# Kernel optimization log

Measured on AMD Instinct MI355X. Metric: run time of the kernel, lower is better.

Reference implementation:

```python
import jax, jax.numpy as jnp
import numpy as np

N = 50000
DIM = 768   # input_dim == feature dim (self.L)
D_ATT = 128 # self.D


def setup_inputs() -> dict:
    key = jax.random.key(0)
    ks = jax.random.split(key, 6)
    s = lambda fan_in: 1.0 / np.sqrt(fan_in)
    return {
        "x": jax.random.normal(ks[0], (1, N, DIM), dtype=jnp.float32),
        "W_feat": jax.random.normal(ks[1], (DIM, DIM), dtype=jnp.float32) * s(DIM),
        "b_feat": jax.random.normal(ks[2], (DIM,), dtype=jnp.float32) * s(DIM),
        "W_a": jax.random.normal(ks[3], (D_ATT, DIM), dtype=jnp.float32) * s(DIM),
        "W_b": jax.random.normal(ks[4], (D_ATT, DIM), dtype=jnp.float32) * s(DIM),
        "W_c": jax.random.normal(ks[5], (1, D_ATT), dtype=jnp.float32) * s(D_ATT),
    }


def reference(x, W_feat, b_feat, W_a, W_b, W_c):
    # x: [1, N, DIM] -> squeeze bag dim -> [N, DIM]
    h = jax.nn.relu(jnp.einsum('nd,ed->ne', x[0], W_feat) + b_feat)  # [N, 768]
    a = jax.nn.relu(jnp.einsum('nd,kd->nk', h, W_a))      # [N, 128]
    b = jax.nn.sigmoid(jnp.einsum('nd,kd->nk', h, W_b))   # [N, 128]
    logits = jnp.einsum('nk,ok->on', a * b, W_c)           # [1, N] (transpose fused)
    A = jax.nn.softmax(logits, axis=-1)                    # [1, N]
    return jnp.einsum('on,nd->od', A, h)                   # [1, 768]
```

## Files before the change

### kernel.cpp

```cpp
#include <hip/hip_runtime.h>
#include <hip/hip_bf16.h>
#include <stdint.h>

#define DEVINL __device__ __forceinline__

using bf16x8 = __attribute__((ext_vector_type(8))) short;
using f32x4  = __attribute__((ext_vector_type(4))) float;

static constexpr int NPTS = 50000;
static constexpr int NPAD = 50176;
static constexpr int DIM  = 768;
static constexpr int DATT = 128;
static constexpr int NRB  = NPAD / 128;

DEVINL ushort f2b(float f) {
  uint32_t u = __float_as_uint(f);
  u += 0x7fffu + ((u >> 16) & 1u);
  return (ushort)(u >> 16);
}
DEVINL float b2f(ushort u) { return __uint_as_float(((uint32_t)u) << 16); }

DEVINL void gload_lds16(const void* g, void* l) {
  __builtin_amdgcn_global_load_lds((const __attribute__((address_space(1))) void*)g,
                                   (__attribute__((address_space(3))) void*)l,
                                   16, 0, 0);
}

DEVINL uint32_t cvtpk(float lo, float hi) {
  union { __hip_bfloat162 h2; uint32_t u; } c;
  c.h2 = __float22bfloat162_rn(float2{lo, hi});
  return c.u;
}
DEVINL bf16x8 pack8(f32x4 lo, f32x4 hi) {
  union { uint32_t u[4]; bf16x8 v; } r;
  r.u[0] = cvtpk(lo[0], lo[1]);
  r.u[1] = cvtpk(lo[2], lo[3]);
  r.u[2] = cvtpk(hi[0], hi[1]);
  r.u[3] = cvtpk(hi[2], hi[3]);
  return r.v;
}

__global__ void cvt_weights_kernel(const float* __restrict__ Wf, const float* __restrict__ Wa,
                                   const float* __restrict__ Wb,
                                   ushort* __restrict__ wfb, ushort* __restrict__ wab,
                                   ushort* __restrict__ wbb) {
  const int NF = DIM * DIM / 8, NA = DATT * DIM / 8;
  int i = blockIdx.x * blockDim.x + threadIdx.x;
  const float* src; ushort* dst; int j;
  if (i < NF)               { src = Wf; dst = wfb; j = i; }
  else if (i < NF + NA)     { src = Wa; dst = wab; j = i - NF; }
  else if (i < NF + 2 * NA) { src = Wb; dst = wbb; j = i - NF - NA; }
  else return;
  const float4* s4 = (const float4*)src;
  float4 v0 = s4[(long)j * 2];
  float4 v1 = s4[(long)j * 2 + 1];
  ushort4 o0 = { f2b(v0.x), f2b(v0.y), f2b(v0.z), f2b(v0.w) };
  ushort4 o1 = { f2b(v1.x), f2b(v1.y), f2b(v1.z), f2b(v1.w) };
  ((ushort4*)dst)[(long)j * 2]     = o0;
  ((ushort4*)dst)[(long)j * 2 + 1] = o1;
}

__global__ __launch_bounds__(512, 2)
void gemm_h_fused(const float* __restrict__ X, const ushort* __restrict__ Wfb,
                  const float* __restrict__ bias, ushort* __restrict__ H) {
  __shared__ char lds[2][65536];

  const int tid  = threadIdx.x;
  const int wid  = tid >> 6;
  const int lane = tid & 63;

  const int bid  = blockIdx.x;
  const int wgid = (bid & 7) * 147 + (bid >> 3);
  const int row0 = (wgid / 3) * 128;
  const int col0 = (wgid % 3) * 256;

  const int wrow = (wid >> 2) * 64;
  const int wcol = (wid & 3) * 64;

  f32x4 acc[4][4] = {};

  const int rA   = wid * 4 + (lane >> 4);
  const int swzA = ((lane & 15) ^ (rA & 7)) * 4;
  const int rB   = wid * 8 + (lane >> 3);
  const int swzB = ((lane & 7) ^ (rB & 7)) * 8;

  auto STAGE = [&](int t, int buf) {
    const int k0 = t * 64;
    char* base = &lds[buf][0];
#pragma unroll
    for (int i = 0; i < 4; ++i) {
      const int r  = i * 32 + rA;
      const int rg = row0 + r;
      const int src = rg < NPTS ? rg : NPTS - 1;
      gload_lds16(X + (long)src * DIM + k0 + swzA, base + (i * 32 + wid * 4) * 256);
    }
#pragma unroll
    for (int i = 0; i < 4; ++i) {
      const int r = i * 64 + rB;
      gload_lds16(Wfb + (long)(col0 + r) * DIM + k0 + swzB,
                  base + 32768 + (i * 64 + wid * 8) * 128);
    }
  };

  auto COMPUTE = [&](int buf) {
    const float*  Ab = (const float*)&lds[buf][0];
    const ushort* Bb = (const ushort*)&lds[buf][32768];
#pragma unroll
    for (int kk = 0; kk < 2; ++kk) {
      const int j = kk * 4 + (lane >> 4);
      bf16x8 a[4];
#pragma unroll
      for (int m = 0; m < 4; ++m) {
        const int ra = wrow + m * 16 + (lane & 15);
        const int s  = ra & 7;
        f32x4 lo = *(const f32x4*)(Ab + ra * 64 + (((2 * j)     ^ s) << 2));
        f32x4 hi = *(const f32x4*)(Ab + ra * 64 + (((2 * j + 1) ^ s) << 2));
        a[m] = pack8(lo, hi);
      }
#pragma unroll
      for (int n = 0; n < 4; ++n) {
        const int rb = wcol + n * 16 + (lane & 15);
        bf16x8 b = *(const bf16x8*)(Bb + rb * 64 + ((j ^ (rb & 7)) << 3));
#pragma unroll
        for (int m = 0; m < 4; ++m)
          acc[m][n] = __builtin_amdgcn_mfma_f32_16x16x32_bf16(a[m], b, acc[m][n], 0, 0, 0);
      }
    }
  };

  STAGE(0, 0);
  asm volatile("s_waitcnt vmcnt(0)" ::: "memory");
  __builtin_amdgcn_s_barrier();
  __builtin_amdgcn_sched_barrier(0);

#pragma unroll 1
  for (int t = 0; t < 12; ++t) {
    if (t < 11) STAGE(t + 1, (t + 1) & 1);
    __builtin_amdgcn_sched_barrier(0);
    COMPUTE(t & 1);
    asm volatile("s_waitcnt vmcnt(0)" ::: "memory");
    __builtin_amdgcn_s_barrier();
    __builtin_amdgcn_sched_barrier(0);
  }

  const int lq = lane >> 4;
  const int lc = lane & 15;
#pragma unroll
  for (int n = 0; n < 4; ++n) {
    const int cg = col0 + wcol + n * 16 + lc;
    const float bv = bias[cg];
#pragma unroll
    for (int m = 0; m < 4; ++m) {
      const int rg = row0 + wrow + m * 16 + lq * 4;
#pragma unroll
      for (int r2 = 0; r2 < 4; ++r2) {
        float v = acc[m][n][r2] + bv;
        v = fmaxf(v, 0.0f);
        H[(long)(rg + r2) * DIM + cg] = f2b(v);
      }
    }
  }
}

__global__ __launch_bounds__(512)
void gate_kernel(const ushort* __restrict__ Hm, const ushort* __restrict__ Wa,
                 const ushort* __restrict__ Wb, const float* __restrict__ Wc,
                 float* __restrict__ logits) {
  __shared__ ushort Hs [128 * 64];
  __shared__ ushort Was[128 * 64];
  __shared__ ushort Wbs[128 * 64];
  const int tid  = threadIdx.x;
  const int wid  = tid >> 6;
  const int lane = tid & 63;
  const int row0 = blockIdx.x * 128;

  f32x4 fa[8] = {};
  f32x4 fb[8] = {};

  const int ld_r = lane >> 3;
  const int ld_c = (lane & 7) * 8;

  for (int k0 = 0; k0 < DIM; k0 += 64) {
    __syncthreads();
#pragma unroll
    for (int i = 0; i < 2; ++i) {
      const int ch = i * 8 + wid;
      const int r  = ch * 8 + ld_r;
      gload_lds16(Hm + (long)(row0 + r) * DIM + k0 + ld_c, Hs  + ch * 512);
      gload_lds16(Wa + (long)r * DIM        + k0 + ld_c, Was + ch * 512);
      gload_lds16(Wb + (long)r * DIM        + k0 + ld_c, Wbs + ch * 512);
    }
    __syncthreads();
#pragma unroll
    for (int kk = 0; kk < 2; ++kk) {
      const int kc = kk * 32 + (lane >> 4) * 8;
      bf16x8 h = *(const bf16x8*)(Hs + (wid * 16 + (lane & 15)) * 64 + kc);
#pragma unroll
      for (int n = 0; n < 8; ++n) {
        bf16x8 wa = *(const bf16x8*)(Was + (n * 16 + (lane & 15)) * 64 + kc);
        bf16x8 wb = *(const bf16x8*)(Wbs + (n * 16 + (lane & 15)) * 64 + kc);
        fa[n] = __builtin_amdgcn_mfma_f32_16x16x32_bf16(h, wa, fa[n], 0, 0, 0);
        fb[n] = __builtin_amdgcn_mfma_f32_16x16x32_bf16(h, wb, fb[n], 0, 0, 0);
      }
    }
  }

  const int lc = lane & 15;
  const int lq = lane >> 4;
  float g[4];
#pragma unroll
  for (int r = 0; r < 4; ++r) {
    float s = 0.f;
#pragma unroll
    for (int n = 0; n < 8; ++n) {
      float av = fmaxf(fa[n][r], 0.f);
      float sg = 1.f / (1.f + expf(-fb[n][r]));
      s += av * sg * Wc[n * 16 + lc];
    }
    s += __shfl_xor(s, 1);
    s += __shfl_xor(s, 2);
    s += __shfl_xor(s, 4);
    s += __shfl_xor(s, 8);
    g[r] = s;
  }
  if (lc == 0) {
    const int rbase = row0 + wid * 16 + lq * 4;
#pragma unroll
    for (int r = 0; r < 4; ++r) {
      const int nidx = rbase + r;
      if (nidx < NPTS) logits[nidx] = g[r];
    }
  }
}

__global__ __launch_bounds__(1024)
void softmax_stats_kernel(const float* __restrict__ logits, float* __restrict__ stats) {
  __shared__ float red[1024];
  const int tid = threadIdx.x;
  float m = -1e30f;
  for (int i = tid; i < NPTS; i += 1024) m = fmaxf(m, logits[i]);
  red[tid] = m; __syncthreads();
  for (int s = 512; s > 0; s >>= 1) {
    if (tid < s) red[tid] = fmaxf(red[tid], red[tid + s]);
    __syncthreads();
  }
  m = red[0];
  __syncthreads();
  float sum = 0.f;
  for (int i = tid; i < NPTS; i += 1024) sum += expf(logits[i] - m);
  red[tid] = sum; __syncthreads();
  for (int s = 512; s > 0; s >>= 1) {
    if (tid < s) red[tid] += red[tid + s];
    __syncthreads();
  }
  if (tid == 0) { stats[0] = m; stats[1] = red[0]; }
}

__global__ __launch_bounds__(192)
void weighted_partial_kernel(const ushort* __restrict__ Hm, const float* __restrict__ logits,
                             const float* __restrict__ stats, float* __restrict__ part) {
  __shared__ float w[128];
  const int b = blockIdx.x, tid = threadIdx.x;
  const int n0 = b * 128;
  if (tid < 128) {
    const int n = n0 + tid;
    w[tid] = (n < NPTS) ? expf(logits[n] - stats[0]) : 0.f;
  }
  __syncthreads();
  float4 acc = {0.f, 0.f, 0.f, 0.f};
  const ushort* hp = Hm + (long)n0 * DIM + tid * 4;
#pragma unroll 4
  for (int r = 0; r < 128; ++r) {
    const float wr = w[r];
    ushort4 v = *(const ushort4*)(hp + (long)r * DIM);
    acc.x += wr * b2f(v.x);
    acc.y += wr * b2f(v.y);
    acc.z += wr * b2f(v.z);
    acc.w += wr * b2f(v.w);
  }
  ((float4*)(part + (long)b * DIM))[tid] = acc;
}

__global__ void final_reduce_kernel(const float* __restrict__ part,
                                    const float* __restrict__ stats,
                                    float* __restrict__ out) {
  const int c = blockIdx.x * blockDim.x + threadIdx.x;
  if (c >= DIM) return;
  float s = 0.f;
  for (int b = 0; b < NRB; ++b) s += part[(long)b * DIM + c];
  out[c] = s / stats[1];
}

extern "C" void kernel_launch(void* const* d_in, const int* in_sizes, int n_in,
                              void* d_out, int out_size, void* d_ws, size_t ws_size,
                              hipStream_t stream) {
  const float* x  = (const float*)d_in[0];
  const float* Wf = (const float*)d_in[1];
  const float* bf = (const float*)d_in[2];
  const float* Wa = (const float*)d_in[3];
  const float* Wb = (const float*)d_in[4];
  const float* Wc = (const float*)d_in[5];
  float* out = (float*)d_out;

  char* p = (char*)d_ws;
  ushort* hb  = (ushort*)p; p += (size_t)NPAD * DIM * 2;
  ushort* wfb = (ushort*)p; p += (size_t)DIM * DIM * 2;
  ushort* wab = (ushort*)p; p += (size_t)DATT * DIM * 2;
  ushort* wbb = (ushort*)p; p += (size_t)DATT * DIM * 2;
  float* logits = (float*)p; p += (size_t)NPAD * 4;
  float* stats  = (float*)p; p += 256;
  float* part   = (float*)p; p += (size_t)NRB * DIM * 4;

  cvt_weights_kernel<<<384, 256, 0, stream>>>(Wf, Wa, Wb, wfb, wab, wbb);

  gemm_h_fused<<<392 * 3, 512, 0, stream>>>(x, wfb, bf, hb);
  gate_kernel<<<NRB, 512, 0, stream>>>(hb, wab, wbb, Wc, logits);
  softmax_stats_kernel<<<1, 1024, 0, stream>>>(logits, stats);
  weighted_partial_kernel<<<NRB, 192, 0, stream>>>(hb, logits, stats, part);
  final_reduce_kernel<<<3, 256, 0, stream>>>(part, stats, out);
}
```

Before: 220.0 us.

## Shrink GEMM tiles with triple-buffered LDS pipeline and parallelize softmax stats

The feature GEMM switches from 128x256 to 128x128 output tiles, doubling the grid, and replaces double buffering with a three-stage LDS ring that keeps two loads in flight using partial vmcnt waits. The single-block softmax statistics kernel is split into a 49-block partial max/sum pass followed by a one-wave combine kernel. The aim is better latency hiding and occupancy in the GEMM and removing a serial bottleneck in the softmax reduction. The trade-off is more A-tile reloads across column tiles, lower MFMA work per LDS read, and one extra kernel launch.

```diff
diff --git a/kernel.cpp b/kernel.cpp
--- a/kernel.cpp
+++ b/kernel.cpp
@@ -12,6 +12,7 @@
 static constexpr int DIM  = 768;
 static constexpr int DATT = 128;
 static constexpr int NRB  = NPAD / 128;
+static constexpr int NSMB = 49;
 
 DEVINL ushort f2b(float f) {
   uint32_t u = __float_as_uint(f);
@@ -60,24 +61,24 @@
   ((ushort4*)dst)[(long)j * 2 + 1] = o1;
 }
 
-__global__ __launch_bounds__(512, 2)
+__global__ __launch_bounds__(512)
 void gemm_h_fused(const float* __restrict__ X, const ushort* __restrict__ Wfb,
                   const float* __restrict__ bias, ushort* __restrict__ H) {
-  __shared__ char lds[2][65536];
+  __shared__ char lds[3][49152];
 
   const int tid  = threadIdx.x;
   const int wid  = tid >> 6;
   const int lane = tid & 63;
 
   const int bid  = blockIdx.x;
-  const int wgid = (bid & 7) * 147 + (bid >> 3);
-  const int row0 = (wgid / 3) * 128;
-  const int col0 = (wgid % 3) * 256;
-
-  const int wrow = (wid >> 2) * 64;
-  const int wcol = (wid & 3) * 64;
-
-  f32x4 acc[4][4] = {};
+  const int wgid = (bid & 7) * 294 + (bid >> 3);
+  const int row0 = (wgid / 6) * 128;
+  const int col0 = (wgid % 6) * 128;
+
+  const int wrow = (wid >> 1) * 32;
+  const int wcol = (wid & 1) * 64;
+
+  f32x4 acc[2][4] = {};
 
   const int rA   = wid * 4 + (lane >> 4);
   const int swzA = ((lane & 15) ^ (rA & 7)) * 4;
@@ -89,13 +90,12 @@
     char* base = &lds[buf][0];
 #pragma unroll
     for (int i = 0; i < 4; ++i) {
-      const int r  = i * 32 + rA;
-      const int rg = row0 + r;
+      const int rg  = row0 + i * 32 + rA;
       const int src = rg < NPTS ? rg : NPTS - 1;
       gload_lds16(X + (long)src * DIM + k0 + swzA, base + (i * 32 + wid * 4) * 256);
     }
 #pragma unroll
-    for (int i = 0; i < 4; ++i) {
+    for (int i = 0; i < 2; ++i) {
       const int r = i * 64 + rB;
       gload_lds16(Wfb + (long)(col0 + r) * DIM + k0 + swzB,
                   base + 32768 + (i * 64 + wid * 8) * 128);
@@ -108,9 +108,9 @@
 #pragma unroll
     for (int kk = 0; kk < 2; ++kk) {
       const int j = kk * 4 + (lane >> 4);
-      bf16x8 a[4];
-#pragma unroll
-      for (int m = 0; m < 4; ++m) {
+      bf16x8 a[2];
+#pragma unroll
+      for (int m = 0; m < 2; ++m) {
         const int ra = wrow + m * 16 + (lane & 15);
         const int s  = ra & 7;
         f32x4 lo = *(const f32x4*)(Ab + ra * 64 + (((2 * j)     ^ s) << 2));
@@ -122,25 +122,32 @@
         const int rb = wcol + n * 16 + (lane & 15);
         bf16x8 b = *(const bf16x8*)(Bb + rb * 64 + ((j ^ (rb & 7)) << 3));
 #pragma unroll
-        for (int m = 0; m < 4; ++m)
+        for (int m = 0; m < 2; ++m)
           acc[m][n] = __builtin_amdgcn_mfma_f32_16x16x32_bf16(a[m], b, acc[m][n], 0, 0, 0);
       }
     }
   };
 
   STAGE(0, 0);
-  asm volatile("s_waitcnt vmcnt(0)" ::: "memory");
-  __builtin_amdgcn_s_barrier();
-  __builtin_amdgcn_sched_barrier(0);
-
+  STAGE(1, 1);
+  int c = 0;
 #pragma unroll 1
   for (int t = 0; t < 12; ++t) {
-    if (t < 11) STAGE(t + 1, (t + 1) & 1);
-    __builtin_amdgcn_sched_barrier(0);
-    COMPUTE(t & 1);
-    asm volatile("s_waitcnt vmcnt(0)" ::: "memory");
+    if (t < 10) {
+      const int nb = (c == 0) ? 2 : c - 1;
+      STAGE(t + 2, nb);
+      asm volatile("s_waitcnt vmcnt(12)" ::: "memory");
+    } else if (t == 10) {
+      asm volatile("s_waitcnt vmcnt(6)" ::: "memory");
+    } else {
+      asm volatile("s_waitcnt vmcnt(0)" ::: "memory");
+    }
     __builtin_amdgcn_s_barrier();
     __builtin_amdgcn_sched_barrier(0);
+    COMPUTE(c);
+    __builtin_amdgcn_sched_barrier(0);
+    __builtin_amdgcn_s_barrier();
+    c = (c == 2) ? 0 : c + 1;
   }
 
   const int lq = lane >> 4;
@@ -150,7 +157,7 @@
     const int cg = col0 + wcol + n * 16 + lc;
     const float bv = bias[cg];
 #pragma unroll
-    for (int m = 0; m < 4; ++m) {
+    for (int m = 0; m < 2; ++m) {
       const int rg = row0 + wrow + m * 16 + lq * 4;
 #pragma unroll
       for (int r2 = 0; r2 < 4; ++r2) {
@@ -234,26 +241,37 @@
 }
 
 __global__ __launch_bounds__(1024)
-void softmax_stats_kernel(const float* __restrict__ logits, float* __restrict__ stats) {
+void softmax_part_kernel(const float* __restrict__ logits, float* __restrict__ part2) {
   __shared__ float red[1024];
   const int tid = threadIdx.x;
-  float m = -1e30f;
-  for (int i = tid; i < NPTS; i += 1024) m = fmaxf(m, logits[i]);
-  red[tid] = m; __syncthreads();
+  const int n = blockIdx.x * 1024 + tid;
+  const float v = (n < NPTS) ? logits[n] : -1e30f;
+  red[tid] = v; __syncthreads();
   for (int s = 512; s > 0; s >>= 1) {
     if (tid < s) red[tid] = fmaxf(red[tid], red[tid + s]);
     __syncthreads();
   }
-  m = red[0];
+  const float m = red[0];
   __syncthreads();
-  float sum = 0.f;
-  for (int i = tid; i < NPTS; i += 1024) sum += expf(logits[i] - m);
-  red[tid] = sum; __syncthreads();
+  red[tid] = (n < NPTS) ? expf(v - m) : 0.f;
+  __syncthreads();
   for (int s = 512; s > 0; s >>= 1) {
     if (tid < s) red[tid] += red[tid + s];
     __syncthreads();
   }
-  if (tid == 0) { stats[0] = m; stats[1] = red[0]; }
+  if (tid == 0) { part2[blockIdx.x * 2] = m; part2[blockIdx.x * 2 + 1] = red[0]; }
+}
+
+__global__ void softmax_comb_kernel(const float* __restrict__ part2,
+                                    float* __restrict__ stats) {
+  const int l = threadIdx.x;
+  float m = (l < NSMB) ? part2[l * 2]     : -1e30f;
+  float s = (l < NSMB) ? part2[l * 2 + 1] : 0.f;
+  float M = m;
+  for (int o = 32; o > 0; o >>= 1) M = fmaxf(M, __shfl_xor(M, o));
+  float sc = s * expf(m - M);
+  for (int o = 32; o > 0; o >>= 1) sc += __shfl_xor(sc, o);
+  if (l == 0) { stats[0] = M; stats[1] = sc; }
 }
 
 __global__ __launch_bounds__(192)
@@ -309,13 +327,15 @@
   ushort* wbb = (ushort*)p; p += (size_t)DATT * DIM * 2;
   float* logits = (float*)p; p += (size_t)NPAD * 4;
   float* stats  = (float*)p; p += 256;
+  float* part2  = (float*)p; p += 1024;
   float* part   = (float*)p; p += (size_t)NRB * DIM * 4;
 
   cvt_weights_kernel<<<384, 256, 0, stream>>>(Wf, Wa, Wb, wfb, wab, wbb);
 
-  gemm_h_fused<<<392 * 3, 512, 0, stream>>>(x, wfb, bf, hb);
+  gemm_h_fused<<<392 * 6, 512, 0, stream>>>(x, wfb, bf, hb);
   gate_kernel<<<NRB, 512, 0, stream>>>(hb, wab, wbb, Wc, logits);
-  softmax_stats_kernel<<<1, 1024, 0, stream>>>(logits, stats);
+  softmax_part_kernel<<<NSMB, 1024, 0, stream>>>(logits, part2);
+  softmax_comb_kernel<<<1, 64, 0, stream>>>(part2, stats);
   weighted_partial_kernel<<<NRB, 192, 0, stream>>>(hb, logits, stats, part);
   final_reduce_kernel<<<3, 256, 0, stream>>>(part, stats, out);
 }
```

After: 244.4 us. 1.11x slower.
